# Kernel tuning notes

Measured on AMD Instinct MI355X. Metric: run time of the kernel, lower is better.

The kernel has to match this reference:

```python
import jax, jax.numpy as jnp
import numpy as np

H = W = 32
C = 384
NH = 12
HEAD = C // NH
SCALE = HEAD ** -0.5
WS = 8            # window size
SS = 4            # shift size
N = WS * WS       # tokens per window (64)
NW = (H // WS) * (W // WS)  # windows per image (16)
HIDDEN = 4 * C
EPS = 1e-5
SQRT_2_OVER_PI = float(np.sqrt(2.0 / np.pi))


def _relative_position_index():
    ch = np.arange(WS)
    coords = np.stack(np.meshgrid(ch, ch, indexing='ij')).reshape(2, -1)  # [2, N]
    rel = (coords[:, :, None] - coords[:, None, :]).transpose(1, 2, 0)    # [N, N, 2]
    rel[:, :, 0] += WS - 1
    rel[:, :, 1] += WS - 1
    rel[:, :, 0] *= 2 * WS - 1
    return rel.sum(-1)  # [N, N] int


def _attn_mask():
    img = np.zeros((H, W), np.float32)
    sl = (slice(0, -WS), slice(-WS, -SS), slice(-SS, None))
    cnt = 0
    for hs in sl:
        for ws_ in sl:
            img[hs, ws_] = cnt
            cnt += 1
    m = img.reshape(H // WS, WS, W // WS, WS).transpose(0, 2, 1, 3).reshape(-1, N)  # [nW, N]
    am = m[:, None, :] - m[:, :, None]
    return np.where(am != 0, -100.0, 0.0).astype(np.float32)  # [nW, N, N]


REL_IDX = jnp.asarray(_relative_position_index())
ATTN_MASK = jnp.asarray(_attn_mask())


def _gelu(x):
    return x * 0.5 * (1.0 + jnp.tanh(SQRT_2_OVER_PI * (x + 0.044715 * x ** 3)))


def _layernorm(x, g, b):
    mu = jnp.mean(x, axis=-1, keepdims=True)
    var = jnp.mean(jnp.square(x - mu), axis=-1, keepdims=True)
    return (x - mu) * jax.lax.rsqrt(var + EPS) * g + b


def _window_partition(x):  # [B,H,W,C] -> [B*nW, N, C]
    B = x.shape[0]
    x = x.reshape(B, H // WS, WS, W // WS, WS, C).transpose(0, 1, 3, 2, 4, 5)
    return x.reshape(-1, N, C)


def _window_reverse(w, B):  # [B*nW, N, C] -> [B,H,W,C]
    x = w.reshape(B, H // WS, W // WS, WS, WS, C).transpose(0, 1, 3, 2, 4, 5)
    return x.reshape(B, H, W, C)


def setup_inputs() -> dict:
    key = jax.random.key(0)
    ks = jax.random.split(key, 16)
    s = 0.02
    return {
        'x': jax.random.normal(ks[0], (32, H * W, C), jnp.float32),
        'norm1_g': jnp.ones((C,), jnp.float32),
        'norm1_b': jnp.zeros((C,), jnp.float32),
        'qkv_w': jax.random.normal(ks[1], (C, 3 * C), jnp.float32) * s,
        'qkv_b': jnp.zeros((3 * C,), jnp.float32),
        'rel_bias_table': jax.random.normal(ks[2], ((2 * WS - 1) ** 2, NH), jnp.float32) * s,
        'proj_w': jax.random.normal(ks[3], (C, C), jnp.float32) * s,
        'proj_b': jnp.zeros((C,), jnp.float32),
        'norm2_g': jnp.ones((C,), jnp.float32),
        'norm2_b': jnp.zeros((C,), jnp.float32),
        'fc1_w': jax.random.normal(ks[4], (C, HIDDEN), jnp.float32) * s,
        'fc1_b': jnp.zeros((HIDDEN,), jnp.float32),
        'fc2_w': jax.random.normal(ks[5], (HIDDEN, C), jnp.float32) * s,
        'fc2_b': jnp.zeros((C,), jnp.float32),
    }


def reference(x, norm1_g, norm1_b, qkv_w, qkv_b, rel_bias_table, proj_w, proj_b,
              norm2_g, norm2_b, fc1_w, fc1_b, fc2_w, fc2_b):
    B = x.shape[0]
    shortcut = x
    y = _layernorm(x, norm1_g, norm1_b).reshape(B, H, W, C)
    y = jnp.roll(y, shift=(-SS, -SS), axis=(1, 2))          # cyclic shift
    win = _window_partition(y)                               # [B*nW, N, C]

    qkv = (win @ qkv_w + qkv_b).reshape(-1, N, 3, NH, HEAD).transpose(2, 0, 3, 1, 4)
    q, k, v = qkv[0], qkv[1], qkv[2]                         # [B*nW, NH, N, HEAD]
    attn = jnp.einsum('whnd,whmd->whnm', q * SCALE, k)       # [B*nW, NH, N, N]

    bias = rel_bias_table[REL_IDX.reshape(-1)].reshape(N, N, NH).transpose(2, 0, 1)
    attn = attn + bias[None]
    attn = attn.reshape(B, NW, NH, N, N) + ATTN_MASK[None, :, None]
    attn = jax.nn.softmax(attn.reshape(-1, NH, N, N), axis=-1)

    out = jnp.einsum('whnm,whmd->wnhd', attn, v).reshape(-1, N, C)
    out = out @ proj_w + proj_b                              # [B*nW, N, C]

    y = _window_reverse(out, B)
    y = jnp.roll(y, shift=(SS, SS), axis=(1, 2)).reshape(B, H * W, C)

    x = shortcut + y                                         # drop_path is identity (eval)
    h = _layernorm(x, norm2_g, norm2_b)
    h = _gelu(h @ fc1_w + fc1_b) @ fc2_w + fc2_b
    return x + h
```

## Files before the change

### kernel.cpp

```cpp
#include <hip/hip_runtime.h>
#include <hip/hip_bf16.h>
#include <math.h>

typedef __hip_bfloat16 bf16;
typedef __attribute__((ext_vector_type(8))) short short8;
typedef __attribute__((ext_vector_type(4))) float floatx4;

static constexpr int TOK = 32768;
static constexpr int CDIM = 384;
static constexpr int HID = 1536;

__device__ __forceinline__ bf16 f2bf(float v) { return __float2bfloat16(v); }

__device__ __forceinline__ unsigned short bf_bits(float a) {
  bf16 h = __float2bfloat16(a);
  unsigned short u;
  __builtin_memcpy(&u, &h, 2);
  return u;
}
__device__ __forceinline__ unsigned pack2(float a, float b) {
  return (unsigned)bf_bits(a) | ((unsigned)bf_bits(b) << 16);
}

typedef const __attribute__((address_space(1))) unsigned gas_t;
typedef __attribute__((address_space(3))) unsigned las_t;
__device__ __forceinline__ void gload16(const bf16* g, const bf16* l) {
  __builtin_amdgcn_global_load_lds((gas_t*)g, (las_t*)l, 16, 0, 0);
}

__global__ __launch_bounds__(256) void k_convt4(
    const float* __restrict__ s0, bf16* __restrict__ d0,
    const float* __restrict__ s1, bf16* __restrict__ d1,
    const float* __restrict__ s2, bf16* __restrict__ d2,
    const float* __restrict__ s3, bf16* __restrict__ d3) {
  int tid = blockIdx.x * 256 + threadIdx.x;
  const float* src; bf16* dst; int Kd, Nd, off;
  if (tid < 442368) { src = s0; dst = d0; Kd = 384; Nd = 1152; off = tid; }
  else if (tid < 589824) { src = s1; dst = d1; Kd = 384; Nd = 384; off = tid - 442368; }
  else if (tid < 1179648) { src = s2; dst = d2; Kd = 384; Nd = 1536; off = tid - 589824; }
  else { src = s3; dst = d3; Kd = 1536; Nd = 384; off = tid - 1179648; }
  int k = off / Nd, n = off - k * Nd;
  dst[(size_t)n * Kd + k] = f2bf(src[off]);
}

__global__ __launch_bounds__(256) void k_ln1(const float* __restrict__ x,
                                             const float* __restrict__ g,
                                             const float* __restrict__ b,
                                             bf16* __restrict__ out) {
  int wt = blockIdx.x * 4 + (threadIdx.x >> 6);
  int lane = threadIdx.x & 63;
  int win = wt >> 6, ntok = wt & 63;
  int bimg = win >> 4, wi = win & 15;
  int sh = (((wi >> 2) << 3) + (ntok >> 3) + 4) & 31;
  int sw = (((wi & 3) << 3) + (ntok & 7) + 4) & 31;
  const float* xr = x + ((size_t)bimg * 1024 + sh * 32 + sw) * CDIM;
  float v[6]; float s = 0.f, ss = 0.f;
#pragma unroll
  for (int j = 0; j < 6; ++j) {
    float t = xr[j * 64 + lane];
    v[j] = t; s += t; ss += t * t;
  }
#pragma unroll
  for (int off = 32; off > 0; off >>= 1) {
    s += __shfl_xor(s, off, 64);
    ss += __shfl_xor(ss, off, 64);
  }
  float mu = s * (1.f / 384.f);
  float var = ss * (1.f / 384.f) - mu * mu;
  float rs = rsqrtf(var + 1e-5f);
  bf16* orow = out + (size_t)wt * CDIM;
#pragma unroll
  for (int j = 0; j < 6; ++j) {
    int c = j * 64 + lane;
    orow[c] = f2bf((v[j] - mu) * rs * g[c] + b[c]);
  }
}

__global__ __launch_bounds__(256) void k_ln2(const float* __restrict__ x1,
                                             const float* __restrict__ g,
                                             const float* __restrict__ b,
                                             bf16* __restrict__ out) {
  int t = blockIdx.x * 4 + (threadIdx.x >> 6);
  int lane = threadIdx.x & 63;
  const float* xr = x1 + (size_t)t * CDIM;
  float v[6]; float s = 0.f, ss = 0.f;
#pragma unroll
  for (int j = 0; j < 6; ++j) {
    float q = xr[j * 64 + lane];
    v[j] = q; s += q; ss += q * q;
  }
#pragma unroll
  for (int off = 32; off > 0; off >>= 1) {
    s += __shfl_xor(s, off, 64);
    ss += __shfl_xor(ss, off, 64);
  }
  float mu = s * (1.f / 384.f);
  float var = ss * (1.f / 384.f) - mu * mu;
  float rs = rsqrtf(var + 1e-5f);
  bf16* orow = out + (size_t)t * CDIM;
#pragma unroll
  for (int j = 0; j < 6; ++j) {
    int c = j * 64 + lane;
    orow[c] = f2bf((v[j] - mu) * rs * g[c] + b[c]);
  }
}

template <int K, int EPI, int NT>
__global__ __launch_bounds__(256) void k_gemm(const bf16* __restrict__ A,
                                              const bf16* __restrict__ Bt,
                                              const float* __restrict__ bias,
                                              const float* __restrict__ extra,
                                              void* __restrict__ outp) {
  __shared__ __attribute__((aligned(16))) char pool[49152];
  bf16* A0 = (bf16*)pool;
  bf16* B0 = (bf16*)(pool + 8192);
  bf16* A1 = (bf16*)(pool + 16384);
  bf16* B1 = (bf16*)(pool + 24576);
  bf16* A2 = (bf16*)(pool + 32768);
  bf16* B2 = (bf16*)(pool + 40960);

  const int tid = threadIdx.x;
  const int wv = tid >> 6, lane = tid & 63;

  const int flat = blockIdx.x;
  const int xcd = flat & 7;
  const int idx = flat >> 3;
  const int rpx = (gridDim.x >> 3) / NT;
  const int cb = idx % NT;
  const int rb = idx / NT;
  const int mblk = (xcd * rpx + rb) * 128, nblk = cb * 128;

  const int srow = lane >> 3;
  const int sc = (lane & 7) ^ srow;
  const int srow2 = 2 * srow + (sc >> 2);
  const int gco = (sc & 3) * 8;
  const bf16* gaw = A + (size_t)(mblk + wv * 32 + srow2) * K + gco;
  const bf16* gbw = Bt + (size_t)(nblk + wv * 32 + srow2) * K + gco;
  bf16* lA0 = A0 + wv * 1024; bf16* lB0 = B0 + wv * 1024;
  bf16* lA1 = A1 + wv * 1024; bf16* lB1 = B1 + wv * 1024;
  bf16* lA2 = A2 + wv * 1024; bf16* lB2 = B2 + wv * 1024;

  const int wr = wv >> 1, wc = wv & 1;
  const int mr = lane & 15, q = lane >> 4;
  const int slot8 = ((((mr & 1) << 2) | q) ^ (mr >> 1)) * 8;
  const int faOff = (wr * 32 + (mr >> 1)) * 64 + slot8;
  const int fbOff = (wc * 32 + (mr >> 1)) * 64 + slot8;

  floatx4 acc[4][4];
#pragma unroll
  for (int i = 0; i < 4; ++i)
#pragma unroll
    for (int j = 0; j < 4; ++j) acc[i][j] = floatx4{0.f, 0.f, 0.f, 0.f};

#define VM4() asm volatile("s_waitcnt vmcnt(4)" ::: "memory")
#define VM0() asm volatile("s_waitcnt vmcnt(0)" ::: "memory")
#define BAR() __builtin_amdgcn_s_barrier()

#define STAGE(LA, LB, KOFF) do { \
    gload16(gaw + (KOFF), (LA)); \
    gload16(gaw + (KOFF) + 16 * K, (LA) + 512); \
    gload16(gbw + (KOFF), (LB)); \
    gload16(gbw + (KOFF) + 16 * K, (LB) + 512); \
  } while (0)

#define COMPUTE(ABASE, BBASE) do { \
    short8 a_[4], b_[4]; \
    _Pragma("unroll") \
    for (int mt = 0; mt < 4; ++mt) a_[mt] = *(const short8*)((ABASE) + faOff + mt * 512); \
    _Pragma("unroll") \
    for (int nt = 0; nt < 4; ++nt) b_[nt] = *(const short8*)((BBASE) + fbOff + nt * 512); \
    _Pragma("unroll") \
    for (int mt = 0; mt < 4; ++mt) \
      _Pragma("unroll") \
      for (int nt = 0; nt < 4; ++nt) \
        acc[mt][nt] = __builtin_amdgcn_mfma_f32_16x16x32_bf16(a_[mt], b_[nt], acc[mt][nt], 0, 0, 0); \
  } while (0)

  STAGE(lA0, lB0, 0);
  STAGE(lA1, lB1, 32);
  for (int k0 = 0; k0 < K - 96; k0 += 96) {
    VM4(); BAR(); STAGE(lA2, lB2, k0 + 64);  COMPUTE(A0, B0);
    VM4(); BAR(); STAGE(lA0, lB0, k0 + 96);  COMPUTE(A1, B1);
    VM4(); BAR(); STAGE(lA1, lB1, k0 + 128); COMPUTE(A2, B2);
  }
  VM4(); BAR(); STAGE(lA2, lB2, K - 32); COMPUTE(A0, B0);
  VM4(); BAR();                          COMPUTE(A1, B1);
  VM0(); BAR();                          COMPUTE(A2, B2);
#undef STAGE
#undef COMPUTE
#undef VM4
#undef VM0
#undef BAR

  __syncthreads();
  float* epsw = (float*)pool + wv * (16 * 68);
  const int rr = lane >> 2, c0 = (lane & 3) * 16;
#pragma unroll
  for (int mt = 0; mt < 4; ++mt) {
#pragma unroll
    for (int nt = 0; nt < 4; ++nt)
#pragma unroll
      for (int r = 0; r < 4; ++r)
        epsw[(q * 4 + r) * 68 + nt * 16 + mr] = acc[mt][nt][r];
    float v[16];
#pragma unroll
    for (int j = 0; j < 4; ++j) {
      float4 t = *(const float4*)&epsw[rr * 68 + c0 + j * 4];
      v[j * 4 + 0] = t.x; v[j * 4 + 1] = t.y; v[j * 4 + 2] = t.z; v[j * 4 + 3] = t.w;
    }
    const int grow = mblk + wr * 64 + mt * 16 + rr;
    const int gcol = nblk + wc * 64 + c0;

    if constexpr (EPI == 0) {
      int win = grow >> 6, ntok = grow & 63;
      int s = gcol / 384;
      int rem = gcol - s * 384;
      int h = rem >> 5, d0 = rem & 31;
      bf16* op = (bf16*)outp + (((size_t)s * 512 + win) * 12 + h) * 2048 + ntok * 32 + d0;
      uint4 pk;
      float bv[16];
#pragma unroll
      for (int j = 0; j < 16; ++j) bv[j] = v[j] + bias[gcol + j];
      pk.x = pack2(bv[0], bv[1]); pk.y = pack2(bv[2], bv[3]);
      pk.z = pack2(bv[4], bv[5]); pk.w = pack2(bv[6], bv[7]);
      *(uint4*)op = pk;
      pk.x = pack2(bv[8], bv[9]); pk.y = pack2(bv[10], bv[11]);
      pk.z = pack2(bv[12], bv[13]); pk.w = pack2(bv[14], bv[15]);
      *(uint4*)(op + 8) = pk;
    } else if constexpr (EPI == 1) {
      int win = grow >> 6, ntok = grow & 63;
      int bimg = win >> 4, wi = win & 15;
      int hh = (((wi >> 2) << 3) + (ntok >> 3) + 4) & 31;
      int ww = (((wi & 3) << 3) + (ntok & 7) + 4) & 31;
      size_t t = (size_t)bimg * 1024 + hh * 32 + ww;
      float* op = (float*)outp + t * CDIM + gcol;
      const float* xr = extra + t * CDIM + gcol;
#pragma unroll
      for (int j = 0; j < 4; ++j) {
        float4 xv = *(const float4*)(xr + j * 4);
        float4 ov;
        ov.x = xv.x + v[j * 4 + 0] + bias[gcol + j * 4 + 0];
        ov.y = xv.y + v[j * 4 + 1] + bias[gcol + j * 4 + 1];
        ov.z = xv.z + v[j * 4 + 2] + bias[gcol + j * 4 + 2];
        ov.w = xv.w + v[j * 4 + 3] + bias[gcol + j * 4 + 3];
        *(float4*)(op + j * 4) = ov;
      }
    }
  }
}

__global__ __launch_bounds__(512, 2) void k_mlp(const bf16* __restrict__ A,
                                                const bf16* __restrict__ W1t,
                                                const bf16* __restrict__ W2t,
                                                const float* __restrict__ b1,
                                                const float* __restrict__ b2,
                                                const float* __restrict__ x1,
                                                float* __restrict__ out) {
  __shared__ __attribute__((aligned(16))) char pool[131072];
  bf16* A0 = (bf16*)pool;
  bf16* A1 = (bf16*)(pool + 8192);
  bf16* A2 = (bf16*)(pool + 16384);
  bf16* W10 = (bf16*)(pool + 24576);
  bf16* W11 = (bf16*)(pool + 32768);
  bf16* W12 = (bf16*)(pool + 40960);
  bf16* hs = (bf16*)(pool + 49152);
  bf16* W2sA = (bf16*)(pool + 81920);
  bf16* W2sB = (bf16*)(pool + 106496);

  const int tid = threadIdx.x;
  const int wv = tid >> 6, lane = tid & 63;
  const int mblk = blockIdx.x * 128;

  const int srow = lane >> 3;
  const int sc = (lane & 7) ^ srow;
  const int srow2 = 2 * srow + (sc >> 2);
  const int gco = (sc & 3) * 8;

  const bf16* ga = A + (size_t)(mblk + wv * 16 + srow2) * 384 + gco;
  const bf16* g1 = W1t + (size_t)(wv * 16 + srow2) * 384 + gco;
  const bf16* g2 = W2t + (size_t)(wv * 48 + srow2) * 1536 + gco;

  const int wr1 = wv >> 2, wc1 = wv & 3;
  const int mr = lane & 15, q = lane >> 4;
  const int slot8 = ((((mr & 1) << 2) | q) ^ (mr >> 1)) * 8;
  const int faOff1 = (wr1 * 32 + (mr >> 1)) * 64 + slot8;
  const int fbOff1 = (wc1 * 16 + (mr >> 1)) * 64 + slot8;
  const int fbOff2 = (wc1 * 48 + (mr >> 1)) * 64 + slot8;
  const size_t hb = (size_t)(wr1 * 64 + mr) * 128;
  int px[4];
#pragma unroll
  for (int kk = 0; kk < 4; ++kk)
    px[kk] = (((kk & 2) << 2) | ((((kk & 1) << 2) | q) ^ (mr & 7))) * 8;

  floatx4 acc1[4][2];
  floatx4 acc2[4][6];
#pragma unroll
  for (int i = 0; i < 4; ++i) {
#pragma unroll
    for (int j = 0; j < 2; ++j) acc1[i][j] = floatx4{0.f, 0.f, 0.f, 0.f};
#pragma unroll
    for (int j = 0; j < 6; ++j) acc2[i][j] = floatx4{0.f, 0.f, 0.f, 0.f};
  }

#define VMW(N) asm volatile("s_waitcnt vmcnt(" #N ")" ::: "memory")
#define BARR() __builtin_amdgcn_s_barrier()
#define ST(ABUF, WBUF, G1P, KO) do { \
    gload16(ga + (KO), (ABUF) + wv * 512); \
    gload16((G1P) + (KO), (WBUF) + wv * 512); \
  } while (0)
#define STW2(BUF, KK) do { \
    _Pragma("unroll") \
    for (int g = 0; g < 3; ++g) \
      gload16(g2 + (KK) * 32 + (size_t)g * 16 * 1536, (BUF) + wv * 1536 + g * 512); \
  } while (0)
#define C1(AB, WB) do { \
    short8 a_[4], b_[2]; \
    _Pragma("unroll") \
    for (int mt = 0; mt < 4; ++mt) a_[mt] = *(const short8*)((AB) + faOff1 + mt * 512); \
    b_[0] = *(const short8*)((WB) + fbOff1); \
    b_[1] = *(const short8*)((WB) + fbOff1 + 512); \
    _Pragma("unroll") \
    for (int mt = 0; mt < 4; ++mt) \
      _Pragma("unroll") \
      for (int nt = 0; nt < 2; ++nt) \
        acc1[mt][nt] = __builtin_amdgcn_mfma_f32_16x16x32_bf16(a_[mt], b_[nt], acc1[mt][nt], 0, 0, 0); \
  } while (0)
#define C2(BUF, KK) do { \
    short8 ha[4], wb[6]; \
    _Pragma("unroll") \
    for (int mt = 0; mt < 4; ++mt) \
      ha[mt] = *(const short8*)(hs + hb + mt * 2048 + px[KK]); \
    _Pragma("unroll") \
    for (int nt = 0; nt < 6; ++nt) \
      wb[nt] = *(const short8*)((BUF) + fbOff2 + nt * 512); \
    _Pragma("unroll") \
    for (int mt = 0; mt < 4; ++mt) \
      _Pragma("unroll") \
      for (int nt = 0; nt < 6; ++nt) \
        acc2[mt][nt] = __builtin_amdgcn_mfma_f32_16x16x32_bf16(ha[mt], wb[nt], acc2[mt][nt], 0, 0, 0); \
  } while (0)

  ST(A0, W10, g1, 0);
  ST(A1, W11, g1, 32);

  for (int ci = 0; ci < 12; ++ci) {
    BARR();
    const int cb = ci * 128;
    float bb0 = b1[cb + wc1 * 32 + mr];
    float bb1 = b1[cb + wc1 * 32 + 16 + mr];
    STW2(W2sA, 0);

    const bf16* g1n = g1 + 49152;
    VMW(5); BARR(); ST(A2, W12, g1, 64);   C1(A0, W10);
    VMW(5); BARR(); ST(A0, W10, g1, 96);   C1(A1, W11);
    VMW(2); BARR(); ST(A1, W11, g1, 128);  C1(A2, W12);
    VMW(2); BARR(); ST(A2, W12, g1, 160);  C1(A0, W10);
    VMW(2); BARR(); ST(A0, W10, g1, 192);  C1(A1, W11);
    VMW(2); BARR(); ST(A1, W11, g1, 224);  C1(A2, W12);
    VMW(2); BARR(); ST(A2, W12, g1, 256);  C1(A0, W10);
    VMW(2); BARR(); ST(A0, W10, g1, 288);  C1(A1, W11);
    VMW(2); BARR(); ST(A1, W11, g1, 320);  C1(A2, W12);
    VMW(2); BARR(); ST(A2, W12, g1, 352);  C1(A0, W10);
    VMW(2); BARR(); ST(A0, W10, g1n, 0);   C1(A1, W11);
    VMW(2); BARR(); ST(A1, W11, g1n, 32);  C1(A2, W12);

#pragma unroll
    for (int mt = 0; mt < 4; ++mt) {
      const int tokb = wr1 * 64 + mt * 16 + q * 4;
#pragma unroll
      for (int nt = 0; nt < 2; ++nt) {
        const float bb = nt ? bb1 : bb0;
        const int sw = wc1 * 4 + nt * 2 + (mr >> 3);
        const int s8 = sw & 8, s7 = sw & 7;
#pragma unroll
        for (int r = 0; r < 4; ++r) {
          float z = acc1[mt][nt][r] + bb;
          float t2 = z * z;
          float cp = __builtin_fmaf(t2, -0.0713548162f, -1.5957691216f);
          float e = __expf(z * cp);
          float gl = z * __builtin_amdgcn_rcpf(1.f + e);
          const int t7 = ((q & 1) << 2) | r;
          hs[(size_t)(tokb + r) * 128 + (s8 | (s7 ^ t7)) * 8 + (mr & 7)] = f2bf(gl);
        }
        acc1[mt][nt] = floatx4{0.f, 0.f, 0.f, 0.f};
      }
    }
    __syncthreads();

    STW2(W2sB, 1);
    C2(W2sA, 0);
    BARR();
    STW2(W2sA, 2);
    VMW(3); BARR();
    C2(W2sB, 1);
    BARR();
    STW2(W2sB, 3);
    VMW(3); BARR();
    C2(W2sA, 2);
    VMW(0); BARR();
    C2(W2sB, 3);

    g1 += 49152;
    g2 += 128;
  }
#undef ST
#undef STW2
#undef C1
#undef C2

  VMW(0);
  __syncthreads();

  float* epsw = (float*)(pool + wv * 6400);
  const int rr = lane >> 2, c4 = (lane & 3) * 24;
#pragma unroll
  for (int mt = 0; mt < 4; ++mt) {
#pragma unroll
    for (int nt = 0; nt < 6; ++nt)
#pragma unroll
      for (int r = 0; r < 4; ++r)
        epsw[(q * 4 + r) * 100 + nt * 16 + mr] = acc2[mt][nt][r];
    const int grow = mblk + wr1 * 64 + mt * 16 + rr;
    const int gcol = wc1 * 96 + c4;
    const float* xr = x1 + (size_t)grow * 384 + gcol;
    float* op = out + (size_t)grow * 384 + gcol;
#pragma unroll
    for (int j = 0; j < 6; ++j) {
      float4 t = *(const float4*)&epsw[rr * 100 + c4 + j * 4];
      float4 xv = *(const float4*)(xr + j * 4);
      float4 bv = *(const float4*)&b2[gcol + j * 4];
      float4 ov;
      ov.x = xv.x + t.x + bv.x;
      ov.y = xv.y + t.y + bv.y;
      ov.z = xv.z + t.z + bv.z;
      ov.w = xv.w + t.w + bv.w;
      *(float4*)(op + j * 4) = ov;
    }
  }
#undef VMW
#undef BARR
}

__global__ __launch_bounds__(64) void k_attn(const bf16* __restrict__ qkv,
                                             const float* __restrict__ tblg,
                                             bf16* __restrict__ out) {
  __shared__ __attribute__((aligned(16))) char pool[16384];
  bf16* Qs = (bf16*)pool;
  bf16* Ks = (bf16*)(pool + 5120);
  bf16* Ps = (bf16*)pool;
  float* Os = (float*)pool;
  bf16* Vt = (bf16*)(pool + 10240);
  unsigned long long* msk = (unsigned long long*)(pool + 14848);
  float* tbl = (float*)(pool + 15360);

  const int bid = blockIdx.x;
  const int win = bid / 12, head = bid - win * 12;
  const int lane = threadIdx.x;
  const int q = lane >> 4, mr = lane & 15;

  for (int i = lane; i < 225; i += 64) tbl[i] = tblg[i * 12 + head];

  size_t base = ((size_t)win * 12 + head) * 2048 + lane * 32;
  const uint4* qp = (const uint4*)(qkv + base);
  const uint4* kp = (const uint4*)(qkv + (size_t)12582912 + base);
  const uint4* vp = (const uint4*)(qkv + (size_t)25165824 + base);
#pragma unroll
  for (int i = 0; i < 4; ++i) *(uint4*)(Qs + lane * 40 + i * 8) = qp[i];
#pragma unroll
  for (int i = 0; i < 4; ++i) *(uint4*)(Ks + lane * 40 + i * 8) = kp[i];
  {
    union { uint4 u[4]; unsigned short h[32]; } vv;
#pragma unroll
    for (int i = 0; i < 4; ++i) vv.u[i] = vp[i];
    unsigned short* VtU = (unsigned short*)Vt;
#pragma unroll
    for (int d = 0; d < 32; ++d) VtU[d * 72 + lane] = vv.h[d];
  }
  {
    int wi = win & 15;
    int ri = lane >> 3, ci = lane & 7;
    int rh = ((wi >> 2) << 3) + ri, rw = ((wi & 3) << 3) + ci;
    int rid = (rh < 24 ? 0 : (rh < 28 ? 1 : 2)) * 3 + (rw < 24 ? 0 : (rw < 28 ? 1 : 2));
    unsigned long long m = 0;
#pragma unroll
    for (int v = 0; v < 9; ++v) {
      unsigned long long bb = __ballot(rid == v);
      if (rid == v) m = bb;
    }
    msk[lane] = m;
  }

  floatx4 sac[4][4];
#pragma unroll
  for (int i = 0; i < 4; ++i)
#pragma unroll
    for (int j = 0; j < 4; ++j) sac[i][j] = floatx4{0.f, 0.f, 0.f, 0.f};
  {
    short8 af[4], bf[4];
#pragma unroll
    for (int t = 0; t < 4; ++t) af[t] = *(const short8*)(Qs + (t * 16 + mr) * 40 + q * 8);
#pragma unroll
    for (int t = 0; t < 4; ++t) bf[t] = *(const short8*)(Ks + (t * 16 + mr) * 40 + q * 8);
#pragma unroll
    for (int mt = 0; mt < 4; ++mt)
#pragma unroll
      for (int nt = 0; nt < 4; ++nt)
        sac[mt][nt] = __builtin_amdgcn_mfma_f32_16x16x32_bf16(af[mt], bf[nt], sac[mt][nt], 0, 0, 0);
  }

  float psum[4][4];
#pragma unroll
  for (int mt = 0; mt < 4; ++mt)
#pragma unroll
    for (int r = 0; r < 4; ++r) psum[mt][r] = 0.f;
#pragma unroll
  for (int mt = 0; mt < 4; ++mt) {
#pragma unroll
    for (int r = 0; r < 4; ++r) {
      const int i = mt * 16 + q * 4 + r;
      const unsigned long long mrow = msk[i];
      const int bi = (i >> 3) * 15 + (i & 7);
#pragma unroll
      for (int nt = 0; nt < 4; ++nt) {
        const int j = nt * 16 + mr;
        const int idx = bi + 112 - (j >> 3) * 15 - (j & 7);
        float val = sac[mt][nt][r] * 0.17677669529663687f + tbl[idx];
        float p = __expf(val);
        p = ((mrow >> j) & 1ull) ? p : 0.f;
        psum[mt][r] += p;
        Ps[i * 72 + j] = f2bf(p);
      }
    }
  }
  float inv[4][4];
#pragma unroll
  for (int mt = 0; mt < 4; ++mt)
#pragma unroll
    for (int r = 0; r < 4; ++r) {
      float s = psum[mt][r];
      s += __shfl_xor(s, 1, 64);
      s += __shfl_xor(s, 2, 64);
      s += __shfl_xor(s, 4, 64);
      s += __shfl_xor(s, 8, 64);
      inv[mt][r] = 1.f / s;
    }

  floatx4 oac[4][2];
#pragma unroll
  for (int i = 0; i < 4; ++i)
#pragma unroll
    for (int j = 0; j < 2; ++j) oac[i][j] = floatx4{0.f, 0.f, 0.f, 0.f};
#pragma unroll
  for (int kk = 0; kk < 2; ++kk) {
    short8 ap[4], bv[2];
#pragma unroll
    for (int mt = 0; mt < 4; ++mt)
      ap[mt] = *(const short8*)(Ps + (mt * 16 + mr) * 72 + kk * 32 + q * 8);
#pragma unroll
    for (int nt = 0; nt < 2; ++nt)
      bv[nt] = *(const short8*)(Vt + (nt * 16 + mr) * 72 + kk * 32 + q * 8);
#pragma unroll
    for (int mt = 0; mt < 4; ++mt)
#pragma unroll
      for (int nt = 0; nt < 2; ++nt)
        oac[mt][nt] = __builtin_amdgcn_mfma_f32_16x16x32_bf16(ap[mt], bv[nt], oac[mt][nt], 0, 0, 0);
  }

#pragma unroll
  for (int mt = 0; mt < 4; ++mt)
#pragma unroll
    for (int nt = 0; nt < 2; ++nt)
#pragma unroll
      for (int r = 0; r < 4; ++r)
        Os[(mt * 16 + q * 4 + r) * 40 + nt * 16 + mr] = oac[mt][nt][r] * inv[mt][r];
  float ov[32];
#pragma unroll
  for (int c = 0; c < 8; ++c) {
    const int cc = c ^ (lane & 7);
    float4 t = *(const float4*)(Os + lane * 40 + cc * 4);
    ov[cc * 4 + 0] = t.x; ov[cc * 4 + 1] = t.y;
    ov[cc * 4 + 2] = t.z; ov[cc * 4 + 3] = t.w;
  }
  uint4* o4 = (uint4*)(out + ((size_t)win * 64 + lane) * CDIM + head * 32);
#pragma unroll
  for (int i = 0; i < 4; ++i) {
    uint4 pk;
    pk.x = pack2(ov[i * 8 + 0], ov[i * 8 + 1]);
    pk.y = pack2(ov[i * 8 + 2], ov[i * 8 + 3]);
    pk.z = pack2(ov[i * 8 + 4], ov[i * 8 + 5]);
    pk.w = pack2(ov[i * 8 + 6], ov[i * 8 + 7]);
    o4[i] = pk;
  }
}

extern "C" void kernel_launch(void* const* d_in, const int* in_sizes, int n_in,
                              void* d_out, int out_size, void* d_ws, size_t ws_size,
                              hipStream_t stream) {
  const float* x = (const float*)d_in[0];
  const float* n1g = (const float*)d_in[1];
  const float* n1b = (const float*)d_in[2];
  const float* qkv_w = (const float*)d_in[3];
  const float* qkv_b = (const float*)d_in[4];
  const float* reltbl = (const float*)d_in[5];
  const float* proj_w = (const float*)d_in[6];
  const float* proj_b = (const float*)d_in[7];
  const float* n2g = (const float*)d_in[8];
  const float* n2b = (const float*)d_in[9];
  const float* fc1_w = (const float*)d_in[10];
  const float* fc1_b = (const float*)d_in[11];
  const float* fc2_w = (const float*)d_in[12];
  const float* fc2_b = (const float*)d_in[13];
  float* out = (float*)d_out;

  char* p = (char*)d_ws;
  bf16* w_qkv_t = (bf16*)p;  p += (size_t)442368 * 2;
  bf16* w_proj_t = (bf16*)p; p += (size_t)147456 * 2;
  bf16* w_fc1_t = (bf16*)p;  p += (size_t)589824 * 2;
  bf16* w_fc2_t = (bf16*)p;  p += (size_t)589824 * 2;
  bf16* bufA = (bf16*)p;     p += (size_t)12582912 * 2;
  bf16* qkvb = (bf16*)p;     p += (size_t)37748736 * 2;
  bf16* attno = (bf16*)p;    p += (size_t)12582912 * 2;
  float* x1 = (float*)p;     p += (size_t)12582912 * 4;

  k_convt4<<<dim3(6912), dim3(256), 0, stream>>>(qkv_w, w_qkv_t, proj_w, w_proj_t,
                                                 fc1_w, w_fc1_t, fc2_w, w_fc2_t);

  k_ln1<<<dim3(8192), dim3(256), 0, stream>>>(x, n1g, n1b, bufA);
  k_gemm<384, 0, 9><<<dim3(9 * 256), dim3(256), 0, stream>>>(bufA, w_qkv_t, qkv_b, nullptr, qkvb);
  k_attn<<<dim3(6144), dim3(64), 0, stream>>>(qkvb, reltbl, attno);
  k_gemm<384, 1, 3><<<dim3(3 * 256), dim3(256), 0, stream>>>(attno, w_proj_t, proj_b, x, x1);
  k_ln2<<<dim3(8192), dim3(256), 0, stream>>>(x1, n2g, n2b, bufA);
  k_mlp<<<dim3(256), dim3(512), 0, stream>>>(bufA, w_fc1_t, w_fc2_t, fc1_b, fc2_b, x1, out);
}
```

Before: 387.4 us.

## Software-pipeline fused MLP: overlap FC2 chunk compute with next FC1 chunk

Restructures the fused FC1+GELU+FC2 loop so the FC2 MFMAs for hidden chunk ci-1 are interleaved with the FC1 k-loop of chunk ci. The W2 slice loads are issued inside the FC1 pipeline, and a drain phase after the loop handles the last chunk. The aim is to hide the serialized FC2 phase and its barriers behind FC1 loads and compute, keeping the matrix units busier. The cost is more complex wait-count bookkeeping and a hidden-activation buffer that must not be overwritten while FC2 still reads it, which adds race risk.

```diff
diff --git a/kernel.cpp b/kernel.cpp
--- a/kernel.cpp
+++ b/kernel.cpp
@@ -303,15 +303,16 @@
   }
 
 #define VMW(N) asm volatile("s_waitcnt vmcnt(" #N ")" ::: "memory")
+#define LGKM0() asm volatile("s_waitcnt lgkmcnt(0)" ::: "memory")
 #define BARR() __builtin_amdgcn_s_barrier()
 #define ST(ABUF, WBUF, G1P, KO) do { \
     gload16(ga + (KO), (ABUF) + wv * 512); \
     gload16((G1P) + (KO), (WBUF) + wv * 512); \
   } while (0)
-#define STW2(BUF, KK) do { \
+#define STW2(BUF, KK, G2P) do { \
     _Pragma("unroll") \
     for (int g = 0; g < 3; ++g) \
-      gload16(g2 + (KK) * 32 + (size_t)g * 16 * 1536, (BUF) + wv * 1536 + g * 512); \
+      gload16((G2P) + (KK) * 32 + (size_t)g * 16 * 1536, (BUF) + wv * 1536 + g * 512); \
   } while (0)
 #define C1(AB, WB) do { \
     short8 a_[4], b_[2]; \
@@ -339,76 +340,92 @@
       for (int nt = 0; nt < 6; ++nt) \
         acc2[mt][nt] = __builtin_amdgcn_mfma_f32_16x16x32_bf16(ha[mt], wb[nt], acc2[mt][nt], 0, 0, 0); \
   } while (0)
-
-  ST(A0, W10, g1, 0);
-  ST(A1, W11, g1, 32);
-
-  for (int ci = 0; ci < 12; ++ci) {
-    BARR();
-    const int cb = ci * 128;
-    float bb0 = b1[cb + wc1 * 32 + mr];
-    float bb1 = b1[cb + wc1 * 32 + 16 + mr];
-    STW2(W2sA, 0);
-
+#define GELU_H(BB0, BB1) do { \
+    _Pragma("unroll") \
+    for (int mt = 0; mt < 4; ++mt) { \
+      const int tokb = wr1 * 64 + mt * 16 + q * 4; \
+      _Pragma("unroll") \
+      for (int nt = 0; nt < 2; ++nt) { \
+        const float bb = nt ? (BB1) : (BB0); \
+        const int sw = wc1 * 4 + nt * 2 + (mr >> 3); \
+        const int s8 = sw & 8, s7 = sw & 7; \
+        _Pragma("unroll") \
+        for (int r = 0; r < 4; ++r) { \
+          float z = acc1[mt][nt][r] + bb; \
+          float t2 = z * z; \
+          float cp = __builtin_fmaf(t2, -0.0713548162f, -1.5957691216f); \
+          float e = __expf(z * cp); \
+          float gl = z * __builtin_amdgcn_rcpf(1.f + e); \
+          const int t7 = ((q & 1) << 2) | r; \
+          hs[(size_t)(tokb + r) * 128 + (s8 | (s7 ^ t7)) * 8 + (mr & 7)] = f2bf(gl); \
+        } \
+        acc1[mt][nt] = floatx4{0.f, 0.f, 0.f, 0.f}; \
+      } \
+    } \
+    LGKM0(); \
+  } while (0)
+
+  {
+    float bb0 = b1[wc1 * 32 + mr];
+    float bb1 = b1[wc1 * 32 + 16 + mr];
+    ST(A0, W10, g1, 0);
+    ST(A1, W11, g1, 32);
     const bf16* g1n = g1 + 49152;
-    VMW(5); BARR(); ST(A2, W12, g1, 64);   C1(A0, W10);
-    VMW(5); BARR(); ST(A0, W10, g1, 96);   C1(A1, W11);
-    VMW(2); BARR(); ST(A1, W11, g1, 128);  C1(A2, W12);
-    VMW(2); BARR(); ST(A2, W12, g1, 160);  C1(A0, W10);
-    VMW(2); BARR(); ST(A0, W10, g1, 192);  C1(A1, W11);
-    VMW(2); BARR(); ST(A1, W11, g1, 224);  C1(A2, W12);
-    VMW(2); BARR(); ST(A2, W12, g1, 256);  C1(A0, W10);
-    VMW(2); BARR(); ST(A0, W10, g1, 288);  C1(A1, W11);
-    VMW(2); BARR(); ST(A1, W11, g1, 320);  C1(A2, W12);
-    VMW(2); BARR(); ST(A2, W12, g1, 352);  C1(A0, W10);
-    VMW(2); BARR(); ST(A0, W10, g1n, 0);   C1(A1, W11);
-    VMW(2); BARR(); ST(A1, W11, g1n, 32);  C1(A2, W12);
-
-#pragma unroll
-    for (int mt = 0; mt < 4; ++mt) {
-      const int tokb = wr1 * 64 + mt * 16 + q * 4;
-#pragma unroll
-      for (int nt = 0; nt < 2; ++nt) {
-        const float bb = nt ? bb1 : bb0;
-        const int sw = wc1 * 4 + nt * 2 + (mr >> 3);
-        const int s8 = sw & 8, s7 = sw & 7;
-#pragma unroll
-        for (int r = 0; r < 4; ++r) {
-          float z = acc1[mt][nt][r] + bb;
-          float t2 = z * z;
-          float cp = __builtin_fmaf(t2, -0.0713548162f, -1.5957691216f);
-          float e = __expf(z * cp);
-          float gl = z * __builtin_amdgcn_rcpf(1.f + e);
-          const int t7 = ((q & 1) << 2) | r;
-          hs[(size_t)(tokb + r) * 128 + (s8 | (s7 ^ t7)) * 8 + (mr & 7)] = f2bf(gl);
-        }
-        acc1[mt][nt] = floatx4{0.f, 0.f, 0.f, 0.f};
-      }
-    }
-    __syncthreads();
-
-    STW2(W2sB, 1);
-    C2(W2sA, 0);
-    BARR();
-    STW2(W2sA, 2);
-    VMW(3); BARR();
-    C2(W2sB, 1);
-    BARR();
-    STW2(W2sB, 3);
-    VMW(3); BARR();
-    C2(W2sA, 2);
-    VMW(0); BARR();
-    C2(W2sB, 3);
-
+    VMW(2); BARR(); ST(A2, W12, g1, 64);                       C1(A0, W10);
+    VMW(2); BARR(); ST(A0, W10, g1, 96);                       C1(A1, W11);
+    VMW(2); BARR(); ST(A1, W11, g1, 128);                      C1(A2, W12);
+    VMW(2); BARR(); ST(A2, W12, g1, 160);                      C1(A0, W10);
+    VMW(2); BARR(); ST(A0, W10, g1, 192);                      C1(A1, W11);
+    VMW(2); BARR(); ST(A1, W11, g1, 224);                      C1(A2, W12);
+    VMW(2); BARR(); ST(A2, W12, g1, 256); STW2(W2sA, 0, g2);   C1(A0, W10);
+    VMW(5); BARR(); ST(A0, W10, g1, 288);                      C1(A1, W11);
+    VMW(5); BARR(); ST(A1, W11, g1, 320); STW2(W2sB, 1, g2);   C1(A2, W12);
+    VMW(5); BARR(); ST(A2, W12, g1, 352);                      C1(A0, W10);
+    VMW(5); BARR(); ST(A0, W10, g1n, 0);                       C1(A1, W11);
+    VMW(2); BARR(); ST(A1, W11, g1n, 32);                      C1(A2, W12);
+    GELU_H(bb0, bb1);
+    g1 += 49152;
+  }
+
+  for (int ci = 1; ci < 12; ++ci) {
+    float bb0 = b1[ci * 128 + wc1 * 32 + mr];
+    float bb1 = b1[ci * 128 + wc1 * 32 + 16 + mr];
+    const bf16* g1n = g1 + 49152;
+    const bf16* g2n = g2 + 128;
+    VMW(4); BARR(); ST(A2, W12, g1, 64);                        C1(A0, W10);
+    VMW(4); BARR(); ST(A0, W10, g1, 96);                        C1(A1, W11); C2(W2sA, 0);
+    VMW(2); BARR(); ST(A1, W11, g1, 128); STW2(W2sA, 2, g2);    C1(A2, W12);
+    VMW(5); BARR(); ST(A2, W12, g1, 160);                       C1(A0, W10); C2(W2sB, 1);
+    VMW(5); BARR(); ST(A0, W10, g1, 192); STW2(W2sB, 3, g2);    C1(A1, W11);
+    VMW(5); BARR(); ST(A1, W11, g1, 224);                       C1(A2, W12); C2(W2sA, 2);
+    VMW(5); BARR(); ST(A2, W12, g1, 256); STW2(W2sA, 0, g2n);   C1(A0, W10);
+    VMW(5); BARR(); ST(A0, W10, g1, 288);                       C1(A1, W11); C2(W2sB, 3);
+    VMW(5); BARR(); ST(A1, W11, g1, 320); STW2(W2sB, 1, g2n);   C1(A2, W12);
+    VMW(5); BARR(); ST(A2, W12, g1, 352);                       C1(A0, W10);
+    VMW(5); BARR(); ST(A0, W10, g1n, 0);                        C1(A1, W11);
+    VMW(2); BARR(); ST(A1, W11, g1n, 32);                       C1(A2, W12);
+    GELU_H(bb0, bb1);
     g1 += 49152;
     g2 += 128;
   }
+
+  VMW(0); BARR();
+  C2(W2sA, 0);
+  BARR();
+  STW2(W2sA, 2, g2);
+  C2(W2sB, 1);
+  BARR();
+  STW2(W2sB, 3, g2);
+  VMW(3); BARR();
+  C2(W2sA, 2);
+  VMW(0); BARR();
+  C2(W2sB, 3);
 #undef ST
 #undef STW2
 #undef C1
 #undef C2
-
-  VMW(0);
+#undef GELU_H
+
   __syncthreads();
 
   float* epsw = (float*)(pool + wv * 6400);
@@ -438,6 +455,7 @@
     }
   }
 #undef VMW
+#undef LGKM0
 #undef BARR
 }
 
```

Result: slower. 396.8 us (+2.4%).
